# Kernel optimization log

Measured on AMD Instinct MI355X. Metric: run time of the kernel, lower is better.

Reference implementation:

```python
import jax, jax.numpy as jnp
import numpy as np

B, S, NX, NH = 4, 2048, 1024, 16
HD = NX // NH
MASKED_BIAS = -10000.0


def setup_inputs() -> dict:
    key = jax.random.key(0)
    k1, k2, k3 = jax.random.split(key, 3)
    return {
        "hidden_states": jax.random.normal(k1, (B, S, NX), dtype=jnp.float32),
        "c_attn_w": jax.random.normal(k2, (NX, 3 * NX), dtype=jnp.float32) * 0.02,
        "c_attn_b": jnp.zeros((3 * NX,), dtype=jnp.float32),
        "c_proj_w": jax.random.normal(k3, (NX, NX), dtype=jnp.float32) * 0.02,
        "c_proj_b": jnp.zeros((NX,), dtype=jnp.float32),
    }


def reference(hidden_states, c_attn_w, c_attn_b, c_proj_w, c_proj_b):
    b, s, nx = hidden_states.shape
    # fused QKV projection (Conv1D == x @ W + b)
    qkv = hidden_states @ c_attn_w + c_attn_b          # [b, s, 3*nx]
    q, k, v = jnp.split(qkv, 3, axis=-1)
    # split heads -> [b, h, s, d]
    q = q.reshape(b, s, NH, HD).transpose(0, 2, 1, 3)
    k = k.reshape(b, s, NH, HD).transpose(0, 2, 1, 3)
    v = v.reshape(b, s, NH, HD).transpose(0, 2, 1, 3)
    # scaled scores [b, h, s, s]
    w = jnp.einsum("bhqd,bhkd->bhqk", q, k) / jnp.float32(np.sqrt(HD))
    # causal mask via torch.where(mask, w, -10000.0) semantics
    causal = jnp.tril(jnp.ones((s, s), dtype=bool))
    w = jnp.where(causal[None, None], w, jnp.float32(MASKED_BIAS))
    w = jax.nn.softmax(w, axis=-1)
    a = jnp.einsum("bhqk,bhkd->bhqd", w, v)            # [b, h, s, d]
    # merge heads
    a = a.transpose(0, 2, 1, 3).reshape(b, s, nx)
    # output projection
    return a @ c_proj_w + c_proj_b
```

## Files before the change

### kernel.cpp

```cpp
#include <hip/hip_runtime.h>


typedef __bf16 bf16_t;
typedef __bf16 bf16x8 __attribute__((ext_vector_type(8)));
typedef __bf16 bf16x4 __attribute__((ext_vector_type(4)));
typedef float  f32x4  __attribute__((ext_vector_type(4)));

#define DI __device__ __forceinline__

static constexpr int Bq = 4, Sq = 2048, NXq = 1024, NHq = 16, HDq = 64;

DI void gl2lds16(const void* g, void* l) {
#if defined(__has_builtin)
#if __has_builtin(__builtin_amdgcn_global_load_lds)
  __builtin_amdgcn_global_load_lds(
      (const __attribute__((address_space(1))) void*)g,
      (__attribute__((address_space(3))) void*)l, 16, 0, 0);
  return;
#endif
#endif
  *(bf16x8*)l = *(const bf16x8*)g;
}

DI float fast_exp2(float x) {
#if defined(__has_builtin)
#if __has_builtin(__builtin_amdgcn_exp2f)
  return __builtin_amdgcn_exp2f(x);
#else
  return exp2f(x);
#endif
#else
  return exp2f(x);
#endif
}

__global__ __launch_bounds__(256) void cvt_bf16(const float* __restrict__ in,
                                                bf16_t* __restrict__ out, int n) {
  int i = (blockIdx.x * 256 + threadIdx.x) * 4;
  if (i >= n) return;
  float4 v = *(const float4*)(in + i);
  bf16x4 o;
  o[0] = (bf16_t)v.x; o[1] = (bf16_t)v.y; o[2] = (bf16_t)v.z; o[3] = (bf16_t)v.w;
  *(bf16x4*)(out + i) = o;
}

__global__ __launch_bounds__(256) void transpose_cvt(const float* __restrict__ in,
                                                     bf16_t* __restrict__ out,
                                                     int R, int C) {
  __shared__ float t[32][33];
  int bx = blockIdx.x * 32, by = blockIdx.y * 32;
  int tx = threadIdx.x, ty = threadIdx.y;
#pragma unroll
  for (int i = 0; i < 32; i += 8)
    t[ty + i][tx] = in[(size_t)(by + ty + i) * C + bx + tx];
  __syncthreads();
#pragma unroll
  for (int i = 0; i < 32; i += 8)
    out[(size_t)(bx + ty + i) * R + by + tx] = (bf16_t)t[tx][ty + i];
}

DI void gemm_main(const bf16_t* __restrict__ A, const bf16_t* __restrict__ Bt,
                  int K, f32x4 acc[4][4], bf16_t* As, bf16_t* Bs,
                  int lane, int w) {
  const int wy = w >> 1, wx = w & 1;
  const int l15 = lane & 15, quad = lane >> 4;
  for (int kt = 0; kt < K; kt += 32) {
    __syncthreads();
#pragma unroll
    for (int i = 0; i < 2; ++i) {
      int g = w * 2 + i;
      int row = g * 16 + (lane >> 2);
      int ko = kt + (lane & 3) * 8;
      gl2lds16(A + (size_t)row * K + ko, As + g * 512 + lane * 8);
      gl2lds16(Bt + (size_t)row * K + ko, Bs + g * 512 + lane * 8);
    }
    __syncthreads();
    bf16x8 af[4], bfr[4];
#pragma unroll
    for (int mi = 0; mi < 4; ++mi)
      af[mi] = *(const bf16x8*)(As + (wy * 64 + mi * 16 + l15) * 32 + quad * 8);
#pragma unroll
    for (int ni = 0; ni < 4; ++ni)
      bfr[ni] = *(const bf16x8*)(Bs + (wx * 64 + ni * 16 + l15) * 32 + quad * 8);
#pragma unroll
    for (int mi = 0; mi < 4; ++mi)
#pragma unroll
      for (int ni = 0; ni < 4; ++ni)
        acc[mi][ni] = __builtin_amdgcn_mfma_f32_16x16x32_bf16(
            af[mi], bfr[ni], acc[mi][ni], 0, 0, 0);
  }
}

__global__ __launch_bounds__(256) void gemm_qkv(
    const bf16_t* __restrict__ X, const bf16_t* __restrict__ Wt,
    const float* __restrict__ bias, bf16_t* __restrict__ qw,
    bf16_t* __restrict__ kw, bf16_t* __restrict__ vtw) {
  __shared__ __align__(16) bf16_t As[128 * 32];
  __shared__ __align__(16) bf16_t Bs[128 * 32];
  const int tid = threadIdx.x, lane = tid & 63, w = tid >> 6;
  const int m0 = blockIdx.y * 128, n0 = blockIdx.x * 128;
  f32x4 acc[4][4];
#pragma unroll
  for (int mi = 0; mi < 4; ++mi)
#pragma unroll
    for (int ni = 0; ni < 4; ++ni) acc[mi][ni] = (f32x4){0.f, 0.f, 0.f, 0.f};
  gemm_main(X + (size_t)m0 * NXq, Wt + (size_t)n0 * NXq, NXq, acc, As, Bs, lane, w);

  const int wy = w >> 1, wx = w & 1, l15 = lane & 15, quad = lane >> 4;
  const float qscale = 0.125f * 1.44269504088896340736f;
#pragma unroll
  for (int mi = 0; mi < 4; ++mi) {
    int rowb = m0 + wy * 64 + mi * 16 + quad * 4;
    int bb = rowb >> 11, sl = rowb & 2047;
#pragma unroll
    for (int ni = 0; ni < 4; ++ni) {
      int col = n0 + wx * 64 + ni * 16 + l15;
      float bv = bias[col];
      f32x4 v = acc[mi][ni];
      int sec = col >> 10;
      int c = col & 1023;
      int h = c >> 6, d = c & 63;
      if (sec == 0) {
#pragma unroll
        for (int r = 0; r < 4; ++r)
          qw[(((size_t)bb * NHq + h) * Sq + sl + r) * HDq + d] =
              (bf16_t)((v[r] + bv) * qscale);
      } else if (sec == 1) {
#pragma unroll
        for (int r = 0; r < 4; ++r)
          kw[(((size_t)bb * NHq + h) * Sq + sl + r) * HDq + d] = (bf16_t)(v[r] + bv);
      } else {
        bf16x4 t;
#pragma unroll
        for (int r = 0; r < 4; ++r) t[r] = (bf16_t)(v[r] + bv);
        *(bf16x4*)(vtw + (((size_t)bb * NHq + h) * HDq + d) * Sq + sl) = t;
      }
    }
  }
}

__global__ __launch_bounds__(256, 4) void attn_fwd(
    const bf16_t* __restrict__ qw, const bf16_t* __restrict__ kw,
    const bf16_t* __restrict__ vtw, bf16_t* __restrict__ aw) {
  __shared__ __align__(16) bf16_t Ks[4096], Vs[4096];
  __shared__ __align__(16) bf16_t Ps[4][32 * 72];
  const int tid = threadIdx.x, lane = tid & 63, w = tid >> 6;
  const int l15 = lane & 15, quad = lane >> 4;

  const int id = blockIdx.x;
  const int bh = ((id & 7) << 3) | ((id >> 3) & 7);
  const int k4 = (id >> 6) & 3, quarter = id >> 8;
  int qtile;
  if (quarter == 0)      qtile = 15 - k4;
  else if (quarter == 1) qtile = 8 + k4;
  else if (quarter == 2) qtile = 7 - k4;
  else                   qtile = k4;
  const int b = bh >> 4, h = bh & 15;

  const bf16_t* Qg = qw + ((size_t)bh * Sq + qtile * 128) * HDq;
  const bf16_t* Kg = kw + (size_t)bh * Sq * HDq;
  const bf16_t* Vg = vtw + (size_t)bh * HDq * Sq;

  bf16x8 qf[2][2];
#pragma unroll
  for (int mi = 0; mi < 2; ++mi)
#pragma unroll
    for (int ks = 0; ks < 2; ++ks)
      qf[mi][ks] = *(const bf16x8*)(
          Qg + (size_t)((w * 2 + mi) * 16 + l15) * HDq + ks * 32 + quad * 8);

  f32x4 o[2][4];
  float lsum[2][4];
#pragma unroll
  for (int mi = 0; mi < 2; ++mi) {
#pragma unroll
    for (int dt = 0; dt < 4; ++dt) o[mi][dt] = (f32x4){0.f, 0.f, 0.f, 0.f};
#pragma unroll
    for (int r = 0; r < 4; ++r) lsum[mi][r] = 0.f;
  }

  bf16_t* Pw = &Ps[w][0];
  const int jmax = 2 * qtile + 2;
  for (int jt = 0; jt < jmax; ++jt) {
    __syncthreads();
#pragma unroll
    for (int i = 0; i < 2; ++i) {
      int u = w * 2 + i, p = u >> 2, g = u & 3;
      gl2lds16(Kg + (size_t)(jt * 64 + g * 16 + (lane >> 2)) * HDq + p * 32 + (lane & 3) * 8,
               Ks + u * 512 + lane * 8);
      gl2lds16(Vg + (size_t)(g * 16 + (lane >> 2)) * Sq + jt * 64 + p * 32 + (lane & 3) * 8,
               Vs + u * 512 + lane * 8);
    }
    __syncthreads();

    f32x4 sc[2][4];
#pragma unroll
    for (int mi = 0; mi < 2; ++mi)
#pragma unroll
      for (int nt = 0; nt < 4; ++nt) sc[mi][nt] = (f32x4){0.f, 0.f, 0.f, 0.f};
#pragma unroll
    for (int ks = 0; ks < 2; ++ks)
#pragma unroll
      for (int nt = 0; nt < 4; ++nt) {
        bf16x8 kf = *(const bf16x8*)(Ks + ks * 2048 + nt * 512 + (l15 * 4 + quad) * 8);
        sc[0][nt] = __builtin_amdgcn_mfma_f32_16x16x32_bf16(qf[0][ks], kf, sc[0][nt], 0, 0, 0);
        sc[1][nt] = __builtin_amdgcn_mfma_f32_16x16x32_bf16(qf[1][ks], kf, sc[1][nt], 0, 0, 0);
      }

    if (jt >= 2 * qtile) {
#pragma unroll
      for (int mi = 0; mi < 2; ++mi) {
        int qrow = qtile * 128 + (w * 2 + mi) * 16 + quad * 4;
#pragma unroll
        for (int nt = 0; nt < 4; ++nt) {
          int key = jt * 64 + nt * 16 + l15;
#pragma unroll
          for (int r = 0; r < 4; ++r)
            if (key > qrow + r) sc[mi][nt][r] = -1e30f;
        }
      }
    }

#pragma unroll
    for (int mi = 0; mi < 2; ++mi)
#pragma unroll
      for (int nt = 0; nt < 4; ++nt)
#pragma unroll
        for (int r = 0; r < 4; ++r) {
          float p = fast_exp2(sc[mi][nt][r]);
          lsum[mi][r] += p;
          Pw[(mi * 16 + quad * 4 + r) * 72 + nt * 16 + l15] = (bf16_t)p;
        }

#pragma unroll
    for (int kk = 0; kk < 2; ++kk) {
      bf16x8 ap0 = *(const bf16x8*)(Pw + (size_t)l15 * 72 + kk * 32 + quad * 8);
      bf16x8 ap1 = *(const bf16x8*)(Pw + (size_t)(16 + l15) * 72 + kk * 32 + quad * 8);
#pragma unroll
      for (int dt = 0; dt < 4; ++dt) {
        bf16x8 bv = *(const bf16x8*)(Vs + kk * 2048 + dt * 512 + (l15 * 4 + quad) * 8);
        o[0][dt] = __builtin_amdgcn_mfma_f32_16x16x32_bf16(ap0, bv, o[0][dt], 0, 0, 0);
        o[1][dt] = __builtin_amdgcn_mfma_f32_16x16x32_bf16(ap1, bv, o[1][dt], 0, 0, 0);
      }
    }
  }

  float linv[2][4];
#pragma unroll
  for (int mi = 0; mi < 2; ++mi)
#pragma unroll
    for (int r = 0; r < 4; ++r) {
      float s = lsum[mi][r];
#pragma unroll
      for (int off = 8; off > 0; off >>= 1) s += __shfl_xor(s, off);
      linv[mi][r] = 1.f / s;
    }

#pragma unroll
  for (int mi = 0; mi < 2; ++mi) {
    int s0 = qtile * 128 + (w * 2 + mi) * 16 + quad * 4;
#pragma unroll
    for (int dt = 0; dt < 4; ++dt) {
      int col = h * 64 + dt * 16 + l15;
#pragma unroll
      for (int r = 0; r < 4; ++r)
        aw[((size_t)b * Sq + s0 + r) * NXq + col] = (bf16_t)(o[mi][dt][r] * linv[mi][r]);
    }
  }
}

__global__ __launch_bounds__(256) void gemm_proj(
    const bf16_t* __restrict__ Aa, const bf16_t* __restrict__ Wt,
    const float* __restrict__ bias, float* __restrict__ out) {
  __shared__ __align__(16) bf16_t As[128 * 32];
  __shared__ __align__(16) bf16_t Bs[128 * 32];
  const int tid = threadIdx.x, lane = tid & 63, w = tid >> 6;
  const int m0 = blockIdx.y * 128, n0 = blockIdx.x * 128;
  f32x4 acc[4][4];
#pragma unroll
  for (int mi = 0; mi < 4; ++mi)
#pragma unroll
    for (int ni = 0; ni < 4; ++ni) acc[mi][ni] = (f32x4){0.f, 0.f, 0.f, 0.f};
  gemm_main(Aa + (size_t)m0 * NXq, Wt + (size_t)n0 * NXq, NXq, acc, As, Bs, lane, w);

  const int wy = w >> 1, wx = w & 1, l15 = lane & 15, quad = lane >> 4;
#pragma unroll
  for (int mi = 0; mi < 4; ++mi) {
    int rowb = m0 + wy * 64 + mi * 16 + quad * 4;
#pragma unroll
    for (int ni = 0; ni < 4; ++ni) {
      int col = n0 + wx * 64 + ni * 16 + l15;
      float bv = bias[col];
#pragma unroll
      for (int r = 0; r < 4; ++r)
        out[(size_t)(rowb + r) * NXq + col] = acc[mi][ni][r] + bv;
    }
  }
}

extern "C" void kernel_launch(void* const* d_in, const int* in_sizes, int n_in,
                              void* d_out, int out_size, void* d_ws, size_t ws_size,
                              hipStream_t stream) {
  const float* hidden   = (const float*)d_in[0];
  const float* c_attn_w = (const float*)d_in[1];
  const float* c_attn_b = (const float*)d_in[2];
  const float* c_proj_w = (const float*)d_in[3];
  const float* c_proj_b = (const float*)d_in[4];
  float* out = (float*)d_out;

  char* ws = (char*)d_ws;
  const size_t szX   = (size_t)8192 * 1024 * 2;
  const size_t szW1  = (size_t)3072 * 1024 * 2;
  const size_t szW2  = (size_t)1024 * 1024 * 2;
  const size_t szQKV = (size_t)Bq * NHq * Sq * HDq * 2;
  bf16_t* Xb  = (bf16_t*)(ws);
  bf16_t* Wt1 = (bf16_t*)(ws + szX);
  bf16_t* Wt2 = (bf16_t*)(ws + szX + szW1);
  bf16_t* qwp = (bf16_t*)(ws + szX + szW1 + szW2);
  bf16_t* kwp = (bf16_t*)(ws + szX + szW1 + szW2 + szQKV);
  bf16_t* vtp = (bf16_t*)(ws + szX + szW1 + szW2 + 2 * szQKV);
  bf16_t* awp = (bf16_t*)(ws + szX + szW1 + szW2 + 3 * szQKV);
  if (ws_size < szX + szW1 + szW2 + 4 * szQKV) return;

  cvt_bf16<<<dim3((8192 * 1024) / (256 * 4)), dim3(256), 0, stream>>>(
      hidden, Xb, 8192 * 1024);
  transpose_cvt<<<dim3(3072 / 32, 1024 / 32), dim3(32, 8), 0, stream>>>(
      c_attn_w, Wt1, 1024, 3072);
  transpose_cvt<<<dim3(1024 / 32, 1024 / 32), dim3(32, 8), 0, stream>>>(
      c_proj_w, Wt2, 1024, 1024);
  gemm_qkv<<<dim3(3072 / 128, 8192 / 128), dim3(256), 0, stream>>>(
      Xb, Wt1, c_attn_b, qwp, kwp, vtp);
  attn_fwd<<<dim3(1024), dim3(256), 0, stream>>>(qwp, kwp, vtp, awp);
  gemm_proj<<<dim3(1024 / 128, 8192 / 128), dim3(256), 0, stream>>>(
      awp, Wt2, c_proj_b, out);
}
```

Baseline: 250.5 us.

## Double GEMM K-tile to 64 and permute V^T layout for vectorized P stores

The shared GEMM main loop now stages a K-slab of 64 instead of 32 per iteration. This halves the number of barrier pairs per tile and issues more loads per sync, at the cost of twice the LDS per block. The V^T written by the QKV GEMM is permuted within each 64-key block. The attention kernel can then pack four P values per row into one bf16x4 LDS store instead of four scalar stores. That write permutation makes the V stores from the QKV epilogue scattered scalar writes, and the attention P·V product relies on the matching key permutation.

```diff
diff --git a/kernel.cpp b/kernel.cpp
--- a/kernel.cpp
+++ b/kernel.cpp
@@ -59,35 +59,40 @@
     out[(size_t)(bx + ty + i) * R + by + tx] = (bf16_t)t[tx][ty + i];
 }
 
-DI void gemm_main(const bf16_t* __restrict__ A, const bf16_t* __restrict__ Bt,
-                  int K, f32x4 acc[4][4], bf16_t* As, bf16_t* Bs,
-                  int lane, int w) {
+DI void gemm_main64(const bf16_t* __restrict__ A, const bf16_t* __restrict__ Bt,
+                    int K, f32x4 acc[4][4], bf16_t* As, bf16_t* Bs,
+                    int lane, int w) {
   const int wy = w >> 1, wx = w & 1;
   const int l15 = lane & 15, quad = lane >> 4;
-  for (int kt = 0; kt < K; kt += 32) {
+  const int sr = lane >> 2, sk = (lane & 3) * 8;
+  for (int kt = 0; kt < K; kt += 64) {
     __syncthreads();
 #pragma unroll
-    for (int i = 0; i < 2; ++i) {
-      int g = w * 2 + i;
-      int row = g * 16 + (lane >> 2);
-      int ko = kt + (lane & 3) * 8;
-      gl2lds16(A + (size_t)row * K + ko, As + g * 512 + lane * 8);
-      gl2lds16(Bt + (size_t)row * K + ko, Bs + g * 512 + lane * 8);
+    for (int i = 0; i < 4; ++i) {
+      int u = w * 4 + i;
+      int p = u >> 3, g = u & 7;
+      int row = g * 16 + sr;
+      int ko = kt + p * 32 + sk;
+      gl2lds16(A + (size_t)row * K + ko, As + u * 512 + lane * 8);
+      gl2lds16(Bt + (size_t)row * K + ko, Bs + u * 512 + lane * 8);
     }
     __syncthreads();
-    bf16x8 af[4], bfr[4];
-#pragma unroll
-    for (int mi = 0; mi < 4; ++mi)
-      af[mi] = *(const bf16x8*)(As + (wy * 64 + mi * 16 + l15) * 32 + quad * 8);
-#pragma unroll
-    for (int ni = 0; ni < 4; ++ni)
-      bfr[ni] = *(const bf16x8*)(Bs + (wx * 64 + ni * 16 + l15) * 32 + quad * 8);
-#pragma unroll
-    for (int mi = 0; mi < 4; ++mi)
+#pragma unroll
+    for (int ks = 0; ks < 2; ++ks) {
+      bf16x8 af[4], bfr[4];
+#pragma unroll
+      for (int mi = 0; mi < 4; ++mi)
+        af[mi] = *(const bf16x8*)(As + ks * 4096 + (wy * 4 + mi) * 512 + l15 * 32 + quad * 8);
 #pragma unroll
       for (int ni = 0; ni < 4; ++ni)
-        acc[mi][ni] = __builtin_amdgcn_mfma_f32_16x16x32_bf16(
-            af[mi], bfr[ni], acc[mi][ni], 0, 0, 0);
+        bfr[ni] = *(const bf16x8*)(Bs + ks * 4096 + (wx * 4 + ni) * 512 + l15 * 32 + quad * 8);
+#pragma unroll
+      for (int mi = 0; mi < 4; ++mi)
+#pragma unroll
+        for (int ni = 0; ni < 4; ++ni)
+          acc[mi][ni] = __builtin_amdgcn_mfma_f32_16x16x32_bf16(
+              af[mi], bfr[ni], acc[mi][ni], 0, 0, 0);
+    }
   }
 }
 
@@ -95,8 +100,8 @@
     const bf16_t* __restrict__ X, const bf16_t* __restrict__ Wt,
     const float* __restrict__ bias, bf16_t* __restrict__ qw,
     bf16_t* __restrict__ kw, bf16_t* __restrict__ vtw) {
-  __shared__ __align__(16) bf16_t As[128 * 32];
-  __shared__ __align__(16) bf16_t Bs[128 * 32];
+  __shared__ __align__(16) bf16_t As[128 * 64];
+  __shared__ __align__(16) bf16_t Bs[128 * 64];
   const int tid = threadIdx.x, lane = tid & 63, w = tid >> 6;
   const int m0 = blockIdx.y * 128, n0 = blockIdx.x * 128;
   f32x4 acc[4][4];
@@ -104,7 +109,7 @@
   for (int mi = 0; mi < 4; ++mi)
 #pragma unroll
     for (int ni = 0; ni < 4; ++ni) acc[mi][ni] = (f32x4){0.f, 0.f, 0.f, 0.f};
-  gemm_main(X + (size_t)m0 * NXq, Wt + (size_t)n0 * NXq, NXq, acc, As, Bs, lane, w);
+  gemm_main64(X + (size_t)m0 * NXq, Wt + (size_t)n0 * NXq, NXq, acc, As, Bs, lane, w);
 
   const int wy = w >> 1, wx = w & 1, l15 = lane & 15, quad = lane >> 4;
   const float qscale = 0.125f * 1.44269504088896340736f;
@@ -130,10 +135,11 @@
         for (int r = 0; r < 4; ++r)
           kw[(((size_t)bb * NHq + h) * Sq + sl + r) * HDq + d] = (bf16_t)(v[r] + bv);
       } else {
-        bf16x4 t;
-#pragma unroll
-        for (int r = 0; r < 4; ++r) t[r] = (bf16_t)(v[r] + bv);
-        *(bf16x4*)(vtw + (((size_t)bb * NHq + h) * HDq + d) * Sq + sl) = t;
+        int sl64 = sl & 63;
+        int pos0 = (sl & ~63) + ((sl64 & 15) << 2) + (sl64 >> 4);
+        bf16_t* vb = vtw + (((size_t)bb * NHq + h) * HDq + d) * Sq + pos0;
+#pragma unroll
+        for (int r = 0; r < 4; ++r) vb[4 * r] = (bf16_t)(v[r] + bv);
       }
     }
   }
@@ -224,13 +230,16 @@
 #pragma unroll
     for (int mi = 0; mi < 2; ++mi)
 #pragma unroll
-      for (int nt = 0; nt < 4; ++nt)
-#pragma unroll
-        for (int r = 0; r < 4; ++r) {
+      for (int r = 0; r < 4; ++r) {
+        bf16x4 pk;
+#pragma unroll
+        for (int nt = 0; nt < 4; ++nt) {
           float p = fast_exp2(sc[mi][nt][r]);
           lsum[mi][r] += p;
-          Pw[(mi * 16 + quad * 4 + r) * 72 + nt * 16 + l15] = (bf16_t)p;
+          pk[nt] = (bf16_t)p;
         }
+        *(bf16x4*)(Pw + (mi * 16 + quad * 4 + r) * 72 + l15 * 4) = pk;
+      }
 
 #pragma unroll
     for (int kk = 0; kk < 2; ++kk) {
@@ -272,8 +281,8 @@
 __global__ __launch_bounds__(256) void gemm_proj(
     const bf16_t* __restrict__ Aa, const bf16_t* __restrict__ Wt,
     const float* __restrict__ bias, float* __restrict__ out) {
-  __shared__ __align__(16) bf16_t As[128 * 32];
-  __shared__ __align__(16) bf16_t Bs[128 * 32];
+  __shared__ __align__(16) bf16_t As[128 * 64];
+  __shared__ __align__(16) bf16_t Bs[128 * 64];
   const int tid = threadIdx.x, lane = tid & 63, w = tid >> 6;
   const int m0 = blockIdx.y * 128, n0 = blockIdx.x * 128;
   f32x4 acc[4][4];
@@ -281,7 +290,7 @@
   for (int mi = 0; mi < 4; ++mi)
 #pragma unroll
     for (int ni = 0; ni < 4; ++ni) acc[mi][ni] = (f32x4){0.f, 0.f, 0.f, 0.f};
-  gemm_main(Aa + (size_t)m0 * NXq, Wt + (size_t)n0 * NXq, NXq, acc, As, Bs, lane, w);
+  gemm_main64(Aa + (size_t)m0 * NXq, Wt + (size_t)n0 * NXq, NXq, acc, As, Bs, lane, w);
 
   const int wy = w >> 1, wx = w & 1, l15 = lane & 15, quad = lane >> 4;
 #pragma unroll
```

New measurement: 266.3 us. +6.3%, slower.

## Double-buffer K/V tiles in LDS to overlap loads with attention compute

Applied to the files above, without the earlier changes.

The attention kernel now keeps two LDS buffers for K and V. It prefetches tile jt+1 with global-to-LDS loads while the MFMA work runs on tile jt, and the first tile is loaded before the loop. This drops one barrier per iteration and hides global load latency behind the score and PV matrix multiplies. In exchange, LDS use per block grows and the launch bound drops from 4 to 3 blocks per CU, so occupancy falls.

```diff
diff --git a/kernel.cpp b/kernel.cpp
--- a/kernel.cpp
+++ b/kernel.cpp
@@ -139,10 +139,10 @@
   }
 }
 
-__global__ __launch_bounds__(256, 4) void attn_fwd(
+__global__ __launch_bounds__(256, 3) void attn_fwd(
     const bf16_t* __restrict__ qw, const bf16_t* __restrict__ kw,
     const bf16_t* __restrict__ vtw, bf16_t* __restrict__ aw) {
-  __shared__ __align__(16) bf16_t Ks[4096], Vs[4096];
+  __shared__ __align__(16) bf16_t Ks[2][4096], Vs[2][4096];
   __shared__ __align__(16) bf16_t Ps[4][32 * 72];
   const int tid = threadIdx.x, lane = tid & 63, w = tid >> 6;
   const int l15 = lane & 15, quad = lane >> 4;
@@ -161,6 +161,15 @@
   const bf16_t* Kg = kw + (size_t)bh * Sq * HDq;
   const bf16_t* Vg = vtw + (size_t)bh * HDq * Sq;
 
+  const int su = w * 2, sr = lane >> 2, sk = (lane & 3) * 8;
+
+#pragma unroll
+  for (int i = 0; i < 2; ++i) {
+    int u = su + i, p = u >> 2, g = u & 3;
+    gl2lds16(Kg + (size_t)(g * 16 + sr) * HDq + p * 32 + sk, Ks[0] + u * 512 + lane * 8);
+    gl2lds16(Vg + (size_t)(g * 16 + sr) * Sq + p * 32 + sk, Vs[0] + u * 512 + lane * 8);
+  }
+
   bf16x8 qf[2][2];
 #pragma unroll
   for (int mi = 0; mi < 2; ++mi)
@@ -182,16 +191,23 @@
   bf16_t* Pw = &Ps[w][0];
   const int jmax = 2 * qtile + 2;
   for (int jt = 0; jt < jmax; ++jt) {
+    const int cur = jt & 1;
     __syncthreads();
-#pragma unroll
-    for (int i = 0; i < 2; ++i) {
-      int u = w * 2 + i, p = u >> 2, g = u & 3;
-      gl2lds16(Kg + (size_t)(jt * 64 + g * 16 + (lane >> 2)) * HDq + p * 32 + (lane & 3) * 8,
-               Ks + u * 512 + lane * 8);
-      gl2lds16(Vg + (size_t)(g * 16 + (lane >> 2)) * Sq + jt * 64 + p * 32 + (lane & 3) * 8,
-               Vs + u * 512 + lane * 8);
-    }
-    __syncthreads();
+
+    if (jt + 1 < jmax) {
+      const int nxt = cur ^ 1;
+#pragma unroll
+      for (int i = 0; i < 2; ++i) {
+        int u = su + i, p = u >> 2, g = u & 3;
+        gl2lds16(Kg + (size_t)((jt + 1) * 64 + g * 16 + sr) * HDq + p * 32 + sk,
+                 Ks[nxt] + u * 512 + lane * 8);
+        gl2lds16(Vg + (size_t)(g * 16 + sr) * Sq + (jt + 1) * 64 + p * 32 + sk,
+                 Vs[nxt] + u * 512 + lane * 8);
+      }
+    }
+
+    const bf16_t* Kc = Ks[cur];
+    const bf16_t* Vc = Vs[cur];
 
     f32x4 sc[2][4];
 #pragma unroll
@@ -202,7 +218,7 @@
     for (int ks = 0; ks < 2; ++ks)
 #pragma unroll
       for (int nt = 0; nt < 4; ++nt) {
-        bf16x8 kf = *(const bf16x8*)(Ks + ks * 2048 + nt * 512 + (l15 * 4 + quad) * 8);
+        bf16x8 kf = *(const bf16x8*)(Kc + ks * 2048 + nt * 512 + (l15 * 4 + quad) * 8);
         sc[0][nt] = __builtin_amdgcn_mfma_f32_16x16x32_bf16(qf[0][ks], kf, sc[0][nt], 0, 0, 0);
         sc[1][nt] = __builtin_amdgcn_mfma_f32_16x16x32_bf16(qf[1][ks], kf, sc[1][nt], 0, 0, 0);
       }
@@ -238,7 +254,7 @@
       bf16x8 ap1 = *(const bf16x8*)(Pw + (size_t)(16 + l15) * 72 + kk * 32 + quad * 8);
 #pragma unroll
       for (int dt = 0; dt < 4; ++dt) {
-        bf16x8 bv = *(const bf16x8*)(Vs + kk * 2048 + dt * 512 + (l15 * 4 + quad) * 8);
+        bf16x8 bv = *(const bf16x8*)(Vc + kk * 2048 + dt * 512 + (l15 * 4 + quad) * 8);
         o[0][dt] = __builtin_amdgcn_mfma_f32_16x16x32_bf16(ap0, bv, o[0][dt], 0, 0, 0);
         o[1][dt] = __builtin_amdgcn_mfma_f32_16x16x32_bf16(ap1, bv, o[1][dt], 0, 0, 0);
       }
```

Measured after the change: 257.4 us. 1.03x slower.
